# Optimization experiments

Hardware: AMD Instinct MI355X
Metric: run time of the kernel (lower is better)

Reference implementation:

```python
import jax, jax.numpy as jnp
import numpy as np

N_PTS = 250000
N_VOX = 60000
D_PT = 256
D_VOX = 256
MID = 256
NUM_CLASS = 20
BN_EPS = 1e-5


def _batchnorm(x, gamma, beta):
    # torch BatchNorm1d in train mode: batch mean / biased variance over dim 0
    mean = jnp.mean(x, axis=0)
    var = jnp.var(x, axis=0)
    return gamma * (x - mean) * jax.lax.rsqrt(var + BN_EPS) + beta


def setup_inputs() -> dict:
    key = jax.random.key(0)
    ks = jax.random.split(key, 8)
    point_feature = jax.random.normal(ks[0], (N_PTS, D_PT), dtype=jnp.float32)
    voxel_feature = jax.random.normal(ks[1], (N_VOX, D_VOX), dtype=jnp.float32)
    p2vmap = jax.random.randint(ks[2], (N_PTS,), 0, N_VOX, dtype=jnp.int64)
    voxel_logits = jax.random.normal(ks[3], (N_VOX, NUM_CLASS), dtype=jnp.float32)
    W1 = jax.random.normal(ks[4], (MID, D_PT + D_VOX), dtype=jnp.float32) * 0.02
    b1 = jnp.zeros((MID,), dtype=jnp.float32)
    W2 = jax.random.normal(ks[5], (MID, D_VOX), dtype=jnp.float32) * 0.02
    b2 = jnp.zeros((MID,), dtype=jnp.float32)
    g1 = jnp.ones((MID,), dtype=jnp.float32)
    be1 = jnp.zeros((MID,), dtype=jnp.float32)
    g2 = jnp.ones((MID,), dtype=jnp.float32)
    be2 = jnp.zeros((MID,), dtype=jnp.float32)
    return {"point_feature": point_feature, "voxel_feature": voxel_feature,
            "voxel_logits": voxel_logits, "W1": W1, "b1": b1, "g1": g1, "be1": be1,
            "W2": W2, "b2": b2, "g2": g2, "be2": be2, "p2vmap": p2vmap}


def reference(point_feature, voxel_feature, voxel_logits, W1, b1, g1, be1,
              W2, b2, g2, be2, p2vmap):
    # gather voxel feature to each point: [N_pts, D_VOX]
    unet_point_feature = voxel_feature[p2vmap]
    x = jnp.concatenate([point_feature, unet_point_feature], axis=1)  # [N_pts, 512]
    x = jax.nn.relu(_batchnorm(x @ W1.T + b1, g1, be1))               # [N_pts, MID]
    cls_prob = jax.nn.softmax(voxel_logits, axis=1)                   # [N_vox, C]
    cls_fea = jnp.einsum('bc,bf->cf', cls_prob, voxel_feature)        # [C, D_VOX]
    cls_fea = _batchnorm(cls_fea @ W2.T + b2, g2, be2)                # [C, MID]
    seg_logits = x @ cls_fea.T                                        # [N_pts, C]
    return seg_logits
```

## Files before the change

### kernel.cpp

```cpp
#include <hip/hip_runtime.h>
#include <hip/hip_bf16.h>

#define N_PTS 250000
#define N_VOX 60000
#define MID   256
#define KDIM  512
#define NCLS  20
#define BN_EPS 1e-5f

typedef __attribute__((ext_vector_type(8))) short short8;
typedef __attribute__((ext_vector_type(4))) float f32x4;
typedef unsigned int u32;

__device__ __forceinline__ unsigned short f2bf_rne(float f) {
    u32 u = __builtin_bit_cast(u32, f);
    u += 0x7FFFu + ((u >> 16) & 1u);
    return (unsigned short)(u >> 16);
}
__device__ __forceinline__ u32 pack2_rnd(float lo, float hi) {
    u32 a = __builtin_bit_cast(u32, lo) + 0x8000u;
    u32 b = __builtin_bit_cast(u32, hi) + 0x8000u;
    return __builtin_amdgcn_perm(b, a, 0x07060302);
}
__device__ __forceinline__ float bfLo(u32 w) { return __builtin_bit_cast(float, w << 16); }
__device__ __forceinline__ float bfHi(u32 w) { return __builtin_bit_cast(float, w & 0xFFFF0000u); }

__device__ __forceinline__ void async_copy16(void* lds, const void* g) {
    __builtin_amdgcn_global_load_lds(
        (const __attribute__((address_space(1))) u32*)g,
        (__attribute__((address_space(3))) u32*)lds, 16, 0, 0);
}

__global__ __launch_bounds__(256) void prep_w1_kernel(
    const float* __restrict__ W1, unsigned short* __restrict__ W1s)
{
    const int idx = blockIdx.x * 256 + threadIdx.x;
    const int lane = idx & 63;
    const int ni = (idx >> 6) & 15;
    const int kt = idx >> 10;
    const int n = ni * 16 + (lane & 15);
    const int k = kt * 32 + (lane >> 4) * 8;
    const float* src = W1 + (size_t)n * 512 + k;
    unsigned short v[8];
    #pragma unroll
    for (int j = 0; j < 8; ++j) v[j] = f2bf_rne(src[j]);
    ushort4* dst = (ushort4*)(W1s + (size_t)idx * 8);
    dst[0] = make_ushort4(v[0], v[1], v[2], v[3]);
    dst[1] = make_ushort4(v[4], v[5], v[6], v[7]);
}

__global__ __launch_bounds__(256, 2) void gemm1_kernel(
    const float* __restrict__ point, const float* __restrict__ vox,
    const unsigned short* __restrict__ W1s, const float* __restrict__ b1,
    const int* __restrict__ p2v,
    unsigned short* __restrict__ hbuf,
    float* __restrict__ colsum, float* __restrict__ colsumsq)
{
    __shared__ float As[2][128 * 32];

    const int tid = threadIdx.x;
    const int bM = blockIdx.x;
    const int lane = tid & 63;
    const int wv = tid >> 6;
    const int wm = wv & 1;
    const int wn = wv >> 1;
    const int l15 = lane & 15;
    const int l4  = lane >> 4;

    const float* aP[4];
    const float* aV[4];
    #pragma unroll
    for (int l = 0; l < 4; ++l) {
        const int idx = l * 256 + tid;
        const int r = idx >> 3;
        const int c = (idx & 7) ^ (r & 7);
        int rg = bM * 128 + r;
        if (rg > N_PTS - 1) rg = N_PTS - 1;
        const int vm = p2v[rg];
        aP[l] = point + (size_t)rg * 256 + c * 4;
        aV[l] = vox   + (size_t)vm * 256 + c * 4;
    }

    f32x4 acc[4][8];
    #pragma unroll
    for (int mi = 0; mi < 4; ++mi)
        #pragma unroll
        for (int j = 0; j < 8; ++j)
            acc[mi][j] = (f32x4){0.f, 0.f, 0.f, 0.f};

    #pragma unroll
    for (int l = 0; l < 4; ++l)
        async_copy16(&As[0][(l * 256 + tid) * 4], aP[l]);

    #pragma unroll 2
    for (int kt = 0; kt < 16; ++kt) {
        __syncthreads();

        short8 bfr[8];
        #pragma unroll
        for (int j = 0; j < 8; ++j) {
            const int ni = wn * 8 + j;
            bfr[j] = *(const short8*)(W1s + ((size_t)(kt * 16 + ni) * 64 + lane) * 8);
        }

        if (kt < 15) {
            const int kn = kt + 1;
            const int ko = (kn & 7) * 32;
            #pragma unroll
            for (int l = 0; l < 4; ++l) {
                const float* src = (kn < 8) ? (aP[l] + ko) : (aV[l] + ko);
                async_copy16(&As[(kn & 1)][(l * 256 + tid) * 4], src);
            }
        }

        const float* buf = As[kt & 1];
        short8 afr[4];
        #pragma unroll
        for (int mi = 0; mi < 4; ++mi) {
            const int m = wm * 64 + mi * 16 + l15;
            const int c0 = (l4 * 2) ^ (m & 7);
            const float* base = buf + m * 32;
            const f32x4 v0 = *(const f32x4*)(base + c0 * 4);
            const f32x4 v1 = *(const f32x4*)(base + (c0 ^ 1) * 4);
            u32 q[4];
            q[0] = pack2_rnd(v0[0], v0[1]);
            q[1] = pack2_rnd(v0[2], v0[3]);
            q[2] = pack2_rnd(v1[0], v1[1]);
            q[3] = pack2_rnd(v1[2], v1[3]);
            u32* ap = (u32*)&afr[mi];
            ap[0] = q[0]; ap[1] = q[1]; ap[2] = q[2]; ap[3] = q[3];
        }

        #pragma unroll
        for (int mi = 0; mi < 4; ++mi)
            #pragma unroll
            for (int j = 0; j < 8; ++j)
                acc[mi][j] = __builtin_amdgcn_mfma_f32_16x16x32_bf16(
                                 afr[mi], bfr[j], acc[mi][j], 0, 0, 0);
    }

    #pragma unroll
    for (int j = 0; j < 8; ++j) {
        const int colG = wn * 128 + j * 16 + l15;
        const float b1v = b1[colG];
        float s = 0.f, sq = 0.f;
        #pragma unroll
        for (int mi = 0; mi < 4; ++mi) {
            const int rgBase = bM * 128 + wm * 64 + mi * 16 + l4 * 4;
            #pragma unroll
            for (int r = 0; r < 4; ++r) {
                const int rr = rgBase + r;
                if (rr < N_PTS) {
                    const float hv = acc[mi][j][r] + b1v;
                    hbuf[(size_t)rr * 256 + colG] = f2bf_rne(hv);
                    s  += hv;
                    sq += hv * hv;
                }
            }
        }
        s  += __shfl_xor(s, 16);  s  += __shfl_xor(s, 32);
        sq += __shfl_xor(sq, 16); sq += __shfl_xor(sq, 32);
        if (lane < 16) {
            atomicAdd(&colsum[colG], s);
            atomicAdd(&colsumsq[colG], sq);
        }
    }
}

#define NCHUNK 938
__global__ __launch_bounds__(256) void cls_acc_kernel(
    const float* __restrict__ logits, const float* __restrict__ vox,
    float* __restrict__ cls_acc)
{
    __shared__ float probs[64 * 24];
    const int tid = threadIdx.x;
    float acc[NCLS];
    #pragma unroll
    for (int c = 0; c < NCLS; ++c) acc[c] = 0.f;

    for (int ci = 0; ci < 4; ++ci) {
        const int chunk = blockIdx.x * 4 + ci;
        if (chunk >= NCHUNK) break;
        const int v0 = chunk * 64;
        __syncthreads();
        if (tid < 64) {
            const int v = v0 + tid;
            if (v < N_VOX) {
                float l[NCLS];
                float mx = -1e30f;
                #pragma unroll
                for (int c = 0; c < NCLS; ++c) {
                    l[c] = logits[(size_t)v * NCLS + c];
                    mx = fmaxf(mx, l[c]);
                }
                float sum = 0.f;
                #pragma unroll
                for (int c = 0; c < NCLS; ++c) { l[c] = __expf(l[c] - mx); sum += l[c]; }
                const float inv = 1.f / sum;
                #pragma unroll
                for (int c = 0; c < NCLS; ++c) probs[tid * 24 + c] = l[c] * inv;
            }
        }
        __syncthreads();
        const int nb = min(64, N_VOX - v0);
        for (int b = 0; b < nb; ++b) {
            const float vv = vox[(size_t)(v0 + b) * 256 + tid];
            #pragma unroll
            for (int c4 = 0; c4 < 5; ++c4) {
                const float4 p = *(const float4*)&probs[b * 24 + c4 * 4];
                acc[c4 * 4 + 0] += p.x * vv;
                acc[c4 * 4 + 1] += p.y * vv;
                acc[c4 * 4 + 2] += p.z * vv;
                acc[c4 * 4 + 3] += p.w * vv;
            }
        }
    }
    #pragma unroll
    for (int c = 0; c < NCLS; ++c)
        atomicAdd(&cls_acc[c * 256 + tid], acc[c]);
}

__global__ __launch_bounds__(256) void fuse_kernel(
    const float* __restrict__ colsum, const float* __restrict__ colsumsq,
    const float* __restrict__ g1, const float* __restrict__ be1,
    float* __restrict__ scl, float* __restrict__ shf,
    const float* __restrict__ cls_acc, const float* __restrict__ W2,
    const float* __restrict__ b2, const float* __restrict__ g2,
    const float* __restrict__ be2, unsigned short* __restrict__ cls_frag)
{
    __shared__ float cf[NCLS * 256];
    __shared__ float cf2[NCLS * 256];
    const int tid = threadIdx.x;

    {
        const float mean = colsum[tid] * (1.0f / N_PTS);
        const float var  = colsumsq[tid] * (1.0f / N_PTS) - mean * mean;
        const float sc = g1[tid] * rsqrtf(var + BN_EPS);
        scl[tid] = sc;
        shf[tid] = be1[tid] - mean * sc;
    }

    for (int i = tid; i < NCLS * 256; i += 256) cf[i] = cls_acc[i];
    __syncthreads();

    float acc[NCLS];
    #pragma unroll
    for (int c = 0; c < NCLS; ++c) acc[c] = b2[tid];
    for (int k = 0; k < 256; k += 4) {
        const float4 w = *(const float4*)&W2[(size_t)tid * 256 + k];
        #pragma unroll
        for (int c = 0; c < NCLS; ++c) {
            const float4 f = *(const float4*)&cf[c * 256 + k];
            acc[c] += w.x * f.x + w.y * f.y + w.z * f.z + w.w * f.w;
        }
    }
    float mean = 0.f;
    #pragma unroll
    for (int c = 0; c < NCLS; ++c) mean += acc[c];
    mean *= (1.f / NCLS);
    float var = 0.f;
    #pragma unroll
    for (int c = 0; c < NCLS; ++c) { const float d = acc[c] - mean; var += d * d; }
    var *= (1.f / NCLS);
    const float sc = g2[tid] * rsqrtf(var + BN_EPS);
    const float bb = be2[tid];
    #pragma unroll
    for (int c = 0; c < NCLS; ++c)
        cf2[c * 256 + tid] = (acc[c] - mean) * sc + bb;
    __syncthreads();

    #pragma unroll
    for (int i = 0; i < 4; ++i) {
        const int idx = i * 256 + tid;
        const int lane = idx & 63;
        const int ni = (idx >> 6) & 1;
        const int kt = idx >> 7;
        const int n = ni * 16 + (lane & 15);
        const int k = kt * 32 + (lane >> 4) * 8;
        unsigned short v[8];
        #pragma unroll
        for (int j = 0; j < 8; ++j)
            v[j] = (n < NCLS) ? f2bf_rne(cf2[n * 256 + k + j]) : (unsigned short)0;
        ushort4* dst = (ushort4*)(cls_frag + (size_t)idx * 8);
        dst[0] = make_ushort4(v[0], v[1], v[2], v[3]);
        dst[1] = make_ushort4(v[4], v[5], v[6], v[7]);
    }
}

__global__ __launch_bounds__(256) void gemm2_kernel(
    const unsigned short* __restrict__ hbuf,
    const float* __restrict__ scl, const float* __restrict__ shf,
    const unsigned short* __restrict__ cls_frag,
    float* __restrict__ out)
{
    __shared__ float sS[256], sT[256];
    const int tid = threadIdx.x;
    sS[tid] = scl[tid];
    sT[tid] = shf[tid];
    __syncthreads();

    const int lane = tid & 63;
    const int w = tid >> 6;
    const int l15 = lane & 15;
    const int l4 = lane >> 4;
    const int mBase = blockIdx.x * 256 + w * 64;

    f32x4 acc[4][2];
    #pragma unroll
    for (int mi = 0; mi < 4; ++mi) {
        acc[mi][0] = (f32x4){0.f, 0.f, 0.f, 0.f};
        acc[mi][1] = (f32x4){0.f, 0.f, 0.f, 0.f};
    }

    #pragma unroll
    for (int kt = 0; kt < 8; ++kt) {
        const int k0 = kt * 32 + l4 * 8;
        const short8 bf0 = *(const short8*)(cls_frag + ((kt * 2 + 0) * 64 + lane) * 8);
        const short8 bf1 = *(const short8*)(cls_frag + ((kt * 2 + 1) * 64 + lane) * 8);
        const f32x4 s0 = *(const f32x4*)&sS[k0];
        const f32x4 s1 = *(const f32x4*)&sS[k0 + 4];
        const f32x4 t0 = *(const f32x4*)&sT[k0];
        const f32x4 t1 = *(const f32x4*)&sT[k0 + 4];
        const float sv[8] = {s0[0], s0[1], s0[2], s0[3], s1[0], s1[1], s1[2], s1[3]};
        const float tv[8] = {t0[0], t0[1], t0[2], t0[3], t1[0], t1[1], t1[2], t1[3]};

        #pragma unroll
        for (int mi = 0; mi < 4; ++mi) {
            int m = mBase + mi * 16 + l15;
            if (m > N_PTS - 1) m = N_PTS - 1;
            const uint4 hx = *(const uint4*)(hbuf + (size_t)m * 256 + k0);
            const u32 wd[4] = {hx.x, hx.y, hx.z, hx.w};
            short8 a;
            u32* ap = (u32*)&a;
            #pragma unroll
            for (int p = 0; p < 4; ++p) {
                const float x0 = fmaxf(fmaf(bfLo(wd[p]), sv[2 * p],     tv[2 * p]),     0.f);
                const float x1 = fmaxf(fmaf(bfHi(wd[p]), sv[2 * p + 1], tv[2 * p + 1]), 0.f);
                ap[p] = pack2_rnd(x0, x1);
            }
            acc[mi][0] = __builtin_amdgcn_mfma_f32_16x16x32_bf16(a, bf0, acc[mi][0], 0, 0, 0);
            acc[mi][1] = __builtin_amdgcn_mfma_f32_16x16x32_bf16(a, bf1, acc[mi][1], 0, 0, 0);
        }
    }

    #pragma unroll
    for (int mi = 0; mi < 4; ++mi) {
        #pragma unroll
        for (int ni = 0; ni < 2; ++ni) {
            const int n = ni * 16 + l15;
            #pragma unroll
            for (int r = 0; r < 4; ++r) {
                const int m = mBase + mi * 16 + l4 * 4 + r;
                if (n < NCLS && m < N_PTS)
                    out[(size_t)m * 20 + n] = acc[mi][ni][r];
            }
        }
    }
}

extern "C" void kernel_launch(void* const* d_in, const int* in_sizes, int n_in,
                              void* d_out, int out_size, void* d_ws, size_t ws_size,
                              hipStream_t stream)
{
    const float* point  = (const float*)d_in[0];
    const float* vox    = (const float*)d_in[1];
    const float* logits = (const float*)d_in[2];
    const float* W1     = (const float*)d_in[3];
    const float* b1     = (const float*)d_in[4];
    const float* g1     = (const float*)d_in[5];
    const float* be1    = (const float*)d_in[6];
    const float* W2     = (const float*)d_in[7];
    const float* b2     = (const float*)d_in[8];
    const float* g2     = (const float*)d_in[9];
    const float* be2    = (const float*)d_in[10];
    const int*   p2v    = (const int*)d_in[11];
    float* out = (float*)d_out;

    char* ws = (char*)d_ws;
    unsigned short* hbuf = (unsigned short*)ws;
    size_t o = (size_t)N_PTS * 256 * 2;
    float* colsum   = (float*)(ws + o); o += 1024;
    float* colsumsq = (float*)(ws + o); o += 1024;
    float* scl      = (float*)(ws + o); o += 1024;
    float* shf      = (float*)(ws + o); o += 1024;
    float* cls_acc  = (float*)(ws + o); o += (size_t)NCLS * 256 * 4;
    unsigned short* W1s      = (unsigned short*)(ws + o); o += (size_t)16384 * 8 * 2;
    unsigned short* cls_frag = (unsigned short*)(ws + o); o += (size_t)1024 * 8 * 2;

    hipMemsetAsync(colsum, 0, 2 * 1024, stream);
    hipMemsetAsync(cls_acc, 0, (size_t)NCLS * 256 * 4, stream);

    prep_w1_kernel<<<64, 256, 0, stream>>>(W1, W1s);
    gemm1_kernel<<<1954, 256, 0, stream>>>(point, vox, W1s, b1, p2v,
                                           hbuf, colsum, colsumsq);
    cls_acc_kernel<<<235, 256, 0, stream>>>(logits, vox, cls_acc);
    fuse_kernel<<<1, 256, 0, stream>>>(colsum, colsumsq, g1, be1, scl, shf,
                                       cls_acc, W2, b2, g2, be2, cls_frag);
    gemm2_kernel<<<977, 256, 0, stream>>>(hbuf, scl, shf, cls_frag, out);
}
```

Before: 669.0 us.

## Precompute voxel half of GEMM1 per voxel and gather projected rows

Splits W1 into point and voxel halves and applies the voxel half once per voxel (60k rows) in a new kernel, storing bf16 results. The point GEMM then does only K=256 and adds the gathered precomputed voxel projection per point. This halves the main GEMM's FLOPs and replaces gathering 256 fp32 voxel features with gathering 256 bf16 values. The change also stages output through LDS for coalesced stores and reduces column statistics in shared memory before global atomics. The voxel contribution is now rounded to bf16 before being added, which slightly changes numerics.

```diff
diff --git a/kernel.cpp b/kernel.cpp
--- a/kernel.cpp
+++ b/kernel.cpp
@@ -4,7 +4,6 @@
 #define N_PTS 250000
 #define N_VOX 60000
 #define MID   256
-#define KDIM  512
 #define NCLS  20
 #define BN_EPS 1e-5f
 
@@ -22,148 +21,249 @@
     u32 b = __builtin_bit_cast(u32, hi) + 0x8000u;
     return __builtin_amdgcn_perm(b, a, 0x07060302);
 }
+__device__ __forceinline__ float bf2f(unsigned short h) {
+    return __builtin_bit_cast(float, ((u32)h) << 16);
+}
 __device__ __forceinline__ float bfLo(u32 w) { return __builtin_bit_cast(float, w << 16); }
 __device__ __forceinline__ float bfHi(u32 w) { return __builtin_bit_cast(float, w & 0xFFFF0000u); }
 
-__device__ __forceinline__ void async_copy16(void* lds, const void* g) {
-    __builtin_amdgcn_global_load_lds(
-        (const __attribute__((address_space(1))) u32*)g,
-        (__attribute__((address_space(3))) u32*)lds, 16, 0, 0);
-}
-
 __global__ __launch_bounds__(256) void prep_w1_kernel(
-    const float* __restrict__ W1, unsigned short* __restrict__ W1s)
+    const float* __restrict__ W1, unsigned short* __restrict__ W1ps,
+    unsigned short* __restrict__ W1vs)
 {
     const int idx = blockIdx.x * 256 + threadIdx.x;
-    const int lane = idx & 63;
-    const int ni = (idx >> 6) & 15;
-    const int kt = idx >> 10;
+    const int half = idx >> 13;
+    const int f = idx & 8191;
+    const int lane = f & 63;
+    const int ni = (f >> 6) & 15;
+    const int kt = f >> 10;
     const int n = ni * 16 + (lane & 15);
-    const int k = kt * 32 + (lane >> 4) * 8;
+    const int k = half * 256 + kt * 32 + (lane >> 4) * 8;
     const float* src = W1 + (size_t)n * 512 + k;
     unsigned short v[8];
     #pragma unroll
     for (int j = 0; j < 8; ++j) v[j] = f2bf_rne(src[j]);
-    ushort4* dst = (ushort4*)(W1s + (size_t)idx * 8);
-    dst[0] = make_ushort4(v[0], v[1], v[2], v[3]);
-    dst[1] = make_ushort4(v[4], v[5], v[6], v[7]);
-}
-
-__global__ __launch_bounds__(256, 2) void gemm1_kernel(
-    const float* __restrict__ point, const float* __restrict__ vox,
-    const unsigned short* __restrict__ W1s, const float* __restrict__ b1,
-    const int* __restrict__ p2v,
-    unsigned short* __restrict__ hbuf,
-    float* __restrict__ colsum, float* __restrict__ colsumsq)
-{
-    __shared__ float As[2][128 * 32];
+    unsigned short* dst = (half ? W1vs : W1ps) + (size_t)f * 8;
+    ((ushort4*)dst)[0] = make_ushort4(v[0], v[1], v[2], v[3]);
+    ((ushort4*)dst)[1] = make_ushort4(v[4], v[5], v[6], v[7]);
+}
+
+__global__ __launch_bounds__(256, 2) void gemm_y_kernel(
+    const float* __restrict__ vox, const unsigned short* __restrict__ W1vs,
+    const float* __restrict__ b1, unsigned short* __restrict__ Ybuf)
+{
+    __shared__ unsigned short Ys[128 * 264];
 
     const int tid = threadIdx.x;
-    const int bM = blockIdx.x;
     const int lane = tid & 63;
     const int wv = tid >> 6;
     const int wm = wv & 1;
     const int wn = wv >> 1;
     const int l15 = lane & 15;
     const int l4  = lane >> 4;
-
-    const float* aP[4];
-    const float* aV[4];
-    #pragma unroll
-    for (int l = 0; l < 4; ++l) {
-        const int idx = l * 256 + tid;
-        const int r = idx >> 3;
-        const int c = (idx & 7) ^ (r & 7);
-        int rg = bM * 128 + r;
-        if (rg > N_PTS - 1) rg = N_PTS - 1;
-        const int vm = p2v[rg];
-        aP[l] = point + (size_t)rg * 256 + c * 4;
-        aV[l] = vox   + (size_t)vm * 256 + c * 4;
+    const int rowBase = blockIdx.x * 128;
+
+    const float* aRow[4];
+    #pragma unroll
+    for (int mi = 0; mi < 4; ++mi) {
+        int rg = rowBase + wm * 64 + mi * 16 + l15;
+        if (rg > N_VOX - 1) rg = N_VOX - 1;
+        aRow[mi] = vox + (size_t)rg * 256 + l4 * 8;
     }
 
     f32x4 acc[4][8];
     #pragma unroll
     for (int mi = 0; mi < 4; ++mi)
         #pragma unroll
+        for (int j = 0; j < 8; ++j) acc[mi][j] = (f32x4){0.f, 0.f, 0.f, 0.f};
+
+    f32x4 arC[4][2], arN[4][2];
+    #pragma unroll
+    for (int mi = 0; mi < 4; ++mi) {
+        arC[mi][0] = *(const f32x4*)(aRow[mi]);
+        arC[mi][1] = *(const f32x4*)(aRow[mi] + 4);
+    }
+
+    #pragma unroll
+    for (int kt = 0; kt < 8; ++kt) {
+        short8 bfr[8];
+        #pragma unroll
         for (int j = 0; j < 8; ++j)
-            acc[mi][j] = (f32x4){0.f, 0.f, 0.f, 0.f};
-
-    #pragma unroll
-    for (int l = 0; l < 4; ++l)
-        async_copy16(&As[0][(l * 256 + tid) * 4], aP[l]);
-
-    #pragma unroll 2
-    for (int kt = 0; kt < 16; ++kt) {
-        __syncthreads();
-
-        short8 bfr[8];
-        #pragma unroll
-        for (int j = 0; j < 8; ++j) {
-            const int ni = wn * 8 + j;
-            bfr[j] = *(const short8*)(W1s + ((size_t)(kt * 16 + ni) * 64 + lane) * 8);
-        }
-
-        if (kt < 15) {
-            const int kn = kt + 1;
-            const int ko = (kn & 7) * 32;
-            #pragma unroll
-            for (int l = 0; l < 4; ++l) {
-                const float* src = (kn < 8) ? (aP[l] + ko) : (aV[l] + ko);
-                async_copy16(&As[(kn & 1)][(l * 256 + tid) * 4], src);
-            }
-        }
-
-        const float* buf = As[kt & 1];
+            bfr[j] = *(const short8*)(W1vs + ((size_t)(kt * 16 + wn * 8 + j) * 64 + lane) * 8);
+        if (kt < 7) {
+            #pragma unroll
+            for (int mi = 0; mi < 4; ++mi) {
+                arN[mi][0] = *(const f32x4*)(aRow[mi] + (kt + 1) * 32);
+                arN[mi][1] = *(const f32x4*)(aRow[mi] + (kt + 1) * 32 + 4);
+            }
+        }
         short8 afr[4];
         #pragma unroll
         for (int mi = 0; mi < 4; ++mi) {
-            const int m = wm * 64 + mi * 16 + l15;
-            const int c0 = (l4 * 2) ^ (m & 7);
-            const float* base = buf + m * 32;
-            const f32x4 v0 = *(const f32x4*)(base + c0 * 4);
-            const f32x4 v1 = *(const f32x4*)(base + (c0 ^ 1) * 4);
-            u32 q[4];
-            q[0] = pack2_rnd(v0[0], v0[1]);
-            q[1] = pack2_rnd(v0[2], v0[3]);
-            q[2] = pack2_rnd(v1[0], v1[1]);
-            q[3] = pack2_rnd(v1[2], v1[3]);
             u32* ap = (u32*)&afr[mi];
-            ap[0] = q[0]; ap[1] = q[1]; ap[2] = q[2]; ap[3] = q[3];
-        }
-
+            ap[0] = pack2_rnd(arC[mi][0][0], arC[mi][0][1]);
+            ap[1] = pack2_rnd(arC[mi][0][2], arC[mi][0][3]);
+            ap[2] = pack2_rnd(arC[mi][1][0], arC[mi][1][1]);
+            ap[3] = pack2_rnd(arC[mi][1][2], arC[mi][1][3]);
+        }
         #pragma unroll
         for (int mi = 0; mi < 4; ++mi)
             #pragma unroll
             for (int j = 0; j < 8; ++j)
                 acc[mi][j] = __builtin_amdgcn_mfma_f32_16x16x32_bf16(
                                  afr[mi], bfr[j], acc[mi][j], 0, 0, 0);
+        #pragma unroll
+        for (int mi = 0; mi < 4; ++mi) { arC[mi][0] = arN[mi][0]; arC[mi][1] = arN[mi][1]; }
     }
 
     #pragma unroll
     for (int j = 0; j < 8; ++j) {
-        const int colG = wn * 128 + j * 16 + l15;
-        const float b1v = b1[colG];
+        const int col = wn * 128 + j * 16 + l15;
+        const float b1v = b1[col];
+        #pragma unroll
+        for (int mi = 0; mi < 4; ++mi)
+            #pragma unroll
+            for (int r = 0; r < 4; ++r) {
+                const int lr = wm * 64 + mi * 16 + l4 * 4 + r;
+                Ys[lr * 264 + col] = f2bf_rne(acc[mi][j][r] + b1v);
+            }
+    }
+    __syncthreads();
+    {
+        const int lr = tid >> 1;
+        const int rg = rowBase + lr;
+        if (rg < N_VOX) {
+            const unsigned short* src = &Ys[lr * 264 + (tid & 1) * 128];
+            unsigned short* dst = Ybuf + (size_t)rg * 256 + (tid & 1) * 128;
+            #pragma unroll
+            for (int i = 0; i < 16; ++i)
+                *(uint4*)(dst + i * 8) = *(const uint4*)(src + i * 8);
+        }
+    }
+}
+
+__global__ __launch_bounds__(256, 2) void gemm1_kernel(
+    const float* __restrict__ point, const unsigned short* __restrict__ W1ps,
+    const unsigned short* __restrict__ Ybuf, const int* __restrict__ p2v,
+    unsigned short* __restrict__ hbuf,
+    float* __restrict__ colsum, float* __restrict__ colsumsq)
+{
+    __shared__ unsigned short Ys[128 * 264];
+    __shared__ float scol[256], ssq[256];
+
+    const int tid = threadIdx.x;
+    scol[tid] = 0.f;
+    ssq[tid] = 0.f;
+
+    const int lane = tid & 63;
+    const int wv = tid >> 6;
+    const int wm = wv & 1;
+    const int wn = wv >> 1;
+    const int l15 = lane & 15;
+    const int l4  = lane >> 4;
+    const int rowBase = blockIdx.x * 128;
+
+    const float* aRow[4];
+    #pragma unroll
+    for (int mi = 0; mi < 4; ++mi) {
+        int rg = rowBase + wm * 64 + mi * 16 + l15;
+        if (rg > N_PTS - 1) rg = N_PTS - 1;
+        aRow[mi] = point + (size_t)rg * 256 + l4 * 8;
+    }
+
+    f32x4 acc[4][8];
+    #pragma unroll
+    for (int mi = 0; mi < 4; ++mi)
+        #pragma unroll
+        for (int j = 0; j < 8; ++j) acc[mi][j] = (f32x4){0.f, 0.f, 0.f, 0.f};
+
+    f32x4 arC[4][2], arN[4][2];
+    #pragma unroll
+    for (int mi = 0; mi < 4; ++mi) {
+        arC[mi][0] = *(const f32x4*)(aRow[mi]);
+        arC[mi][1] = *(const f32x4*)(aRow[mi] + 4);
+    }
+
+    #pragma unroll
+    for (int kt = 0; kt < 8; ++kt) {
+        short8 bfr[8];
+        #pragma unroll
+        for (int j = 0; j < 8; ++j)
+            bfr[j] = *(const short8*)(W1ps + ((size_t)(kt * 16 + wn * 8 + j) * 64 + lane) * 8);
+        if (kt < 7) {
+            #pragma unroll
+            for (int mi = 0; mi < 4; ++mi) {
+                arN[mi][0] = *(const f32x4*)(aRow[mi] + (kt + 1) * 32);
+                arN[mi][1] = *(const f32x4*)(aRow[mi] + (kt + 1) * 32 + 4);
+            }
+        }
+        short8 afr[4];
+        #pragma unroll
+        for (int mi = 0; mi < 4; ++mi) {
+            u32* ap = (u32*)&afr[mi];
+            ap[0] = pack2_rnd(arC[mi][0][0], arC[mi][0][1]);
+            ap[1] = pack2_rnd(arC[mi][0][2], arC[mi][0][3]);
+            ap[2] = pack2_rnd(arC[mi][1][0], arC[mi][1][1]);
+            ap[3] = pack2_rnd(arC[mi][1][2], arC[mi][1][3]);
+        }
+        #pragma unroll
+        for (int mi = 0; mi < 4; ++mi)
+            #pragma unroll
+            for (int j = 0; j < 8; ++j)
+                acc[mi][j] = __builtin_amdgcn_mfma_f32_16x16x32_bf16(
+                                 afr[mi], bfr[j], acc[mi][j], 0, 0, 0);
+        #pragma unroll
+        for (int mi = 0; mi < 4; ++mi) { arC[mi][0] = arN[mi][0]; arC[mi][1] = arN[mi][1]; }
+    }
+
+    {
+        const int lr = tid >> 1;
+        int rg = rowBase + lr;
+        if (rg > N_PTS - 1) rg = N_PTS - 1;
+        const unsigned short* ysrc = Ybuf + (size_t)p2v[rg] * 256 + (tid & 1) * 128;
+        unsigned short* ydst = &Ys[lr * 264 + (tid & 1) * 128];
+        #pragma unroll
+        for (int i = 0; i < 16; ++i)
+            *(uint4*)(ydst + i * 8) = *(const uint4*)(ysrc + i * 8);
+    }
+    __syncthreads();
+
+    #pragma unroll
+    for (int j = 0; j < 8; ++j) {
+        const int col = wn * 128 + j * 16 + l15;
         float s = 0.f, sq = 0.f;
         #pragma unroll
         for (int mi = 0; mi < 4; ++mi) {
-            const int rgBase = bM * 128 + wm * 64 + mi * 16 + l4 * 4;
             #pragma unroll
             for (int r = 0; r < 4; ++r) {
-                const int rr = rgBase + r;
-                if (rr < N_PTS) {
-                    const float hv = acc[mi][j][r] + b1v;
-                    hbuf[(size_t)rr * 256 + colG] = f2bf_rne(hv);
-                    s  += hv;
-                    sq += hv * hv;
-                }
+                const int lr = wm * 64 + mi * 16 + l4 * 4 + r;
+                unsigned short* p = &Ys[lr * 264 + col];
+                const float hv = acc[mi][j][r] + bf2f(*p);
+                *p = f2bf_rne(hv);
+                if (rowBase + lr < N_PTS) { s += hv; sq += hv * hv; }
             }
         }
         s  += __shfl_xor(s, 16);  s  += __shfl_xor(s, 32);
         sq += __shfl_xor(sq, 16); sq += __shfl_xor(sq, 32);
-        if (lane < 16) {
-            atomicAdd(&colsum[colG], s);
-            atomicAdd(&colsumsq[colG], sq);
-        }
+        if (l4 == 0) {
+            atomicAdd(&scol[col], s);
+            atomicAdd(&ssq[col], sq);
+        }
+    }
+    __syncthreads();
+
+    {
+        const int lr = tid >> 1;
+        const int rg = rowBase + lr;
+        if (rg < N_PTS) {
+            const unsigned short* src = &Ys[lr * 264 + (tid & 1) * 128];
+            unsigned short* dst = hbuf + (size_t)rg * 256 + (tid & 1) * 128;
+            #pragma unroll
+            for (int i = 0; i < 16; ++i)
+                *(uint4*)(dst + i * 8) = *(const uint4*)(src + i * 8);
+        }
+        atomicAdd(&colsum[tid], scol[tid]);
+        atomicAdd(&colsumsq[tid], ssq[tid]);
     }
 }
 
@@ -344,7 +444,7 @@
     }
 
     #pragma unroll
-    for (int mi = 0; mi < 4; ++mi) {
+    for (int mi = 0; mi < 4; ++mi)
         #pragma unroll
         for (int ni = 0; ni < 2; ++ni) {
             const int n = ni * 16 + l15;
@@ -355,7 +455,6 @@
                     out[(size_t)m * 20 + n] = acc[mi][ni][r];
             }
         }
-    }
 }
 
 extern "C" void kernel_launch(void* const* d_in, const int* in_sizes, int n_in,
@@ -379,19 +478,22 @@
     char* ws = (char*)d_ws;
     unsigned short* hbuf = (unsigned short*)ws;
     size_t o = (size_t)N_PTS * 256 * 2;
+    unsigned short* Ybuf = (unsigned short*)(ws + o); o += (size_t)N_VOX * 256 * 2;
     float* colsum   = (float*)(ws + o); o += 1024;
     float* colsumsq = (float*)(ws + o); o += 1024;
     float* scl      = (float*)(ws + o); o += 1024;
     float* shf      = (float*)(ws + o); o += 1024;
     float* cls_acc  = (float*)(ws + o); o += (size_t)NCLS * 256 * 4;
-    unsigned short* W1s      = (unsigned short*)(ws + o); o += (size_t)16384 * 8 * 2;
+    unsigned short* W1ps     = (unsigned short*)(ws + o); o += (size_t)8192 * 8 * 2;
+    unsigned short* W1vs     = (unsigned short*)(ws + o); o += (size_t)8192 * 8 * 2;
     unsigned short* cls_frag = (unsigned short*)(ws + o); o += (size_t)1024 * 8 * 2;
 
     hipMemsetAsync(colsum, 0, 2 * 1024, stream);
     hipMemsetAsync(cls_acc, 0, (size_t)NCLS * 256 * 4, stream);
 
-    prep_w1_kernel<<<64, 256, 0, stream>>>(W1, W1s);
-    gemm1_kernel<<<1954, 256, 0, stream>>>(point, vox, W1s, b1, p2v,
+    prep_w1_kernel<<<64, 256, 0, stream>>>(W1, W1ps, W1vs);
+    gemm_y_kernel<<<469, 256, 0, stream>>>(vox, W1vs, b1, Ybuf);
+    gemm1_kernel<<<1954, 256, 0, stream>>>(point, W1ps, Ybuf, p2v,
                                            hbuf, colsum, colsumsq);
     cls_acc_kernel<<<235, 256, 0, stream>>>(logits, vox, cls_acc);
     fuse_kernel<<<1, 256, 0, stream>>>(colsum, colsumsq, g1, be1, scl, shf,
```

After: 676.0 us. Within noise of the previous version (+1.0%).
